# Kernel optimization log

Hardware: AMD Instinct MI355X
Metric: run time of the kernel (lower is better)

## Reference

```python
import jax, jax.numpy as jnp
import numpy as np
from jax import lax

B, NQ, DQ, DKV = 4, 256, 256, 256
H_IMG, W_IMG = 256, 256
HEADS, DH, TOPW, WS, FACTOR = 8, 32, 4, 8, 2
INNER = HEADS * DH
DOUT = 256


def _ln(x, g, b, eps=1e-5):
    mu = x.mean(-1, keepdims=True)
    var = ((x - mu) ** 2).mean(-1, keepdims=True)
    return (x - mu) * lax.rsqrt(var + eps) * g + b


def _softmax_one(x, axis):
    x = x - x.max(axis=axis, keepdims=True)
    e = jnp.exp(x)
    return e / (1.0 + e.sum(axis=axis, keepdims=True))


def setup_inputs():
    key = jax.random.key(0)
    ks = jax.random.split(key, 10)
    s = 0.02
    return {
        'query': jax.random.normal(ks[0], (B, NQ, DQ), jnp.float32),
        'image': jax.random.normal(ks[1], (B, DKV, H_IMG, W_IMG), jnp.float32),
        'conv_w': jax.random.normal(ks[2], (INNER, DKV, FACTOR, FACTOR), jnp.float32) * s,
        'conv_b': jnp.zeros((INNER,), jnp.float32),
        'key_pos_embed': jax.random.normal(ks[3], (1, TOPW * WS * WS, INNER), jnp.float32),
        'normq_g': jnp.ones((DQ,), jnp.float32),
        'normq_b': jnp.zeros((DQ,), jnp.float32),
        'normkv_g': jnp.ones((INNER,), jnp.float32),
        'normkv_b': jnp.zeros((INNER,), jnp.float32),
        'wq': jax.random.normal(ks[4], (INNER, DQ), jnp.float32) * s,
        'wk': jax.random.normal(ks[5], (INNER, INNER), jnp.float32) * s,
        'wv': jax.random.normal(ks[6], (INNER, INNER), jnp.float32) * s,
        'w_rec': jax.random.normal(ks[7], (DQ, INNER), jnp.float32) * s,
        'mlp_g': jnp.ones((DQ,), jnp.float32),
        'mlp_b': jnp.zeros((DQ,), jnp.float32),
        'mlp_w1': jax.random.normal(ks[8], (DOUT, DQ), jnp.float32) * s,
        'mlp_b1': jnp.zeros((DOUT,), jnp.float32),
        'mlp_w2': jax.random.normal(ks[9], (DOUT, DOUT), jnp.float32) * s,
        'mlp_b2': jnp.zeros((DOUT,), jnp.float32),
    }


def reference(query, image, conv_w, conv_b, key_pos_embed, normq_g, normq_b,
              normkv_g, normkv_b, wq, wk, wv, w_rec, mlp_g, mlp_b,
              mlp_w1, mlp_b1, mlp_w2, mlp_b2):
    # 1) patchify image: Conv2d(dim_kv -> inner_dim, k=factor, s=factor)
    imagec = lax.conv_general_dilated(image, conv_w, (FACTOR, FACTOR), 'VALID',
                                      dimension_numbers=('NCHW', 'OIHW', 'NCHW'))
    imagec = imagec + conv_b[None, :, None, None]
    b, c, H, W = imagec.shape
    M, N = H // WS, W // WS  # number of windows per axis
    # einops 'b c (h m) (w n) -> (b m n) (h w) c' with h=w=WS -> DILATED windows
    x = imagec.reshape(b, c, WS, M, WS, N).transpose(0, 3, 5, 2, 4, 1)
    x = x.reshape(b * M * N, WS * WS, c)  # (bMN, ws^2, inner)
    # 2) double softmax_one window pooling
    cor = jnp.einsum('wpc,wqc->wpq', x, x) * (DKV ** -0.5)
    cor = _softmax_one(cor, -1).sum(axis=1)          # (bMN, ws^2)
    cor = _softmax_one(cor, -1)[..., None]           # (bMN, ws^2, 1)
    imagew = (x * cor).sum(axis=1).reshape(b, M * N, c)  # window summaries
    # 3) query projection + top-w window routing (non-differentiable)
    q = _ln(query, normq_g, normq_b) @ wq.T          # (b, Nq, inner)
    rattn = jnp.einsum('bqc,bmc->bqm', lax.stop_gradient(q),
                       lax.stop_gradient(imagew)) * (INNER ** -0.5)
    topw_idx = lax.top_k(rattn, TOPW)[1]             # (b, Nq, topw)
    # 4) gather proposal KV windows
    win_kv = x.reshape(b, M * N, WS * WS, c)
    props = jax.vmap(lambda img, idx: img[idx])(win_kv, topw_idx)  # (b,Nq,topw,ws^2,c)
    nq = q.shape[1]
    props = props.reshape(b * nq, TOPW * WS * WS, c) + key_pos_embed
    # 5) per-query single-token attention over topw*ws^2 keys
    kv = _ln(props, normkv_g, normkv_b)
    k = (kv @ wk.T).reshape(b * nq, -1, HEADS, DH)
    v = (kv @ wv.T).reshape(b * nq, -1, HEADS, DH)
    qh = q.reshape(b * nq, HEADS, DH)
    dots = jnp.einsum('bgc,bngc->bgn', qh, k) * (DH ** -0.5)
    attn = jax.nn.softmax(dots, axis=-1)
    out = jnp.einsum('bgn,bngc->bgc', attn, v).reshape(b, nq, INNER)
    out = out @ w_rec.T + query
    # 6) residual MLP (LN -> Linear -> ReLU -> Linear)
    h = _ln(out, mlp_g, mlp_b)
    h = jax.nn.relu(h @ mlp_w1.T + mlp_b1) @ mlp_w2.T + mlp_b2
    return out + h
```

## Files before the change

kernel.cpp:

```cpp
#include <hip/hip_runtime.h>
#include <math.h>


typedef __bf16 bf16x8_t __attribute__((ext_vector_type(8)));
typedef float f32x4 __attribute__((ext_vector_type(4)));
typedef unsigned short ushortx8 __attribute__((ext_vector_type(8)));
typedef unsigned short ushortx4 __attribute__((ext_vector_type(4)));

__device__ __forceinline__ unsigned short f2bf(float f) {
  unsigned int u = __float_as_uint(f);
  unsigned int r = (u + 0x7FFFu + ((u >> 16) & 1u)) >> 16;
  return (unsigned short)r;
}
__device__ __forceinline__ float bf2f(unsigned short h) {
  return __uint_as_float(((unsigned int)h) << 16);
}

#define MFMA16(a, b, c) \
  __builtin_amdgcn_mfma_f32_16x16x32_bf16( \
      __builtin_bit_cast(bf16x8_t, (a)), __builtin_bit_cast(bf16x8_t, (b)), (c), 0, 0, 0)

__global__ __launch_bounds__(256) void k_prepw(
    const float* __restrict__ cw, unsigned short* __restrict__ cwh,
    unsigned short* __restrict__ cwl)
{
  const int o = blockIdx.x;
  const int k4 = threadIdx.x * 4;
  const float4 w = *(const float4*)(cw + (size_t)o * 1024 + k4);
  float f[4] = {w.x, w.y, w.z, w.w};
  ushortx4 h, l;
#pragma unroll
  for (int i = 0; i < 4; ++i) {
    h[i] = f2bf(f[i]);
    l[i] = f2bf(f[i] - bf2f(h[i]));
  }
  *(ushortx4*)(cwh + (size_t)o * 1024 + k4) = h;
  *(ushortx4*)(cwl + (size_t)o * 1024 + k4) = l;
}

__global__ __launch_bounds__(512, 4) void k_conv(
    const float* __restrict__ img, const unsigned short* __restrict__ cwh,
    const unsigned short* __restrict__ cwl, const float* __restrict__ cb,
    float* __restrict__ x)
{
  __shared__ unsigned short Ah[128 * 40];
  __shared__ unsigned short Al[128 * 40];
  __shared__ unsigned short Bh[128 * 40];
  __shared__ unsigned short Bl[128 * 40];

  const int tid = threadIdx.x;
  const int blk = blockIdx.x;
  const int nh = blk & 1, by = blk >> 1;
  const int b = by >> 7, y = by & 127;
  const int n0 = nh * 128;

  const int lane = tid & 63, wid = tid >> 6;
  const int wr = wid >> 2, wc = wid & 3;
  const int lr = lane & 15, lk = lane >> 4;

  const int ax = tid & 127, aq = tid >> 7;
  const float* abase = img + (size_t)b * 16777216 + (size_t)(2 * y) * 256 + 2 * ax;
  const int bo = tid >> 2, bkq = tid & 3;

  f32x4 acc[4][2];
#pragma unroll
  for (int i = 0; i < 4; ++i)
#pragma unroll
    for (int j = 0; j < 2; ++j) acc[i][j] = (f32x4){0.f, 0.f, 0.f, 0.f};

  for (int kc = 0; kc < 32; ++kc) {
    __syncthreads();
    {
      float f[8];
#pragma unroll
      for (int cc = 0; cc < 2; ++cc) {
        const int cin = kc * 8 + aq * 2 + cc;
        const float* p = abase + (size_t)cin * 65536;
        const float2 v0 = *(const float2*)p;
        const float2 v1 = *(const float2*)(p + 256);
        f[cc * 4 + 0] = v0.x; f[cc * 4 + 1] = v0.y;
        f[cc * 4 + 2] = v1.x; f[cc * 4 + 3] = v1.y;
      }
      ushortx8 h, l;
#pragma unroll
      for (int i = 0; i < 8; ++i) {
        h[i] = f2bf(f[i]);
        l[i] = f2bf(f[i] - bf2f(h[i]));
      }
      *(ushortx8*)&Ah[ax * 40 + aq * 8] = h;
      *(ushortx8*)&Al[ax * 40 + aq * 8] = l;
    }
    {
      const size_t goff = (size_t)(n0 + bo) * 1024 + kc * 32 + bkq * 8;
      *(ushortx8*)&Bh[bo * 40 + bkq * 8] = *(const ushortx8*)(cwh + goff);
      *(ushortx8*)&Bl[bo * 40 + bkq * 8] = *(const ushortx8*)(cwl + goff);
    }
    __syncthreads();
    ushortx8 bh2[2], bl2[2];
#pragma unroll
    for (int ni = 0; ni < 2; ++ni) {
      const int col = wc * 32 + ni * 16 + lr;
      bh2[ni] = *(ushortx8*)&Bh[col * 40 + lk * 8];
      bl2[ni] = *(ushortx8*)&Bl[col * 40 + lk * 8];
    }
#pragma unroll
    for (int mi = 0; mi < 4; ++mi) {
      const int row = wr * 64 + mi * 16 + lr;
      const ushortx8 ah = *(ushortx8*)&Ah[row * 40 + lk * 8];
      const ushortx8 al = *(ushortx8*)&Al[row * 40 + lk * 8];
#pragma unroll
      for (int ni = 0; ni < 2; ++ni) {
        acc[mi][ni] = MFMA16(ah, bh2[ni], acc[mi][ni]);
        acc[mi][ni] = MFMA16(al, bh2[ni], acc[mi][ni]);
        acc[mi][ni] = MFMA16(ah, bl2[ni], acc[mi][ni]);
      }
    }
  }
  const int hh = y >> 4, mm = y & 15;
#pragma unroll
  for (int mi = 0; mi < 4; ++mi) {
    const int pbase = wr * 64 + mi * 16 + lk * 4;
#pragma unroll
    for (int ni = 0; ni < 2; ++ni) {
      const int c = n0 + wc * 32 + ni * 16 + lr;
      const float cbv = cb[c];
#pragma unroll
      for (int r = 0; r < 4; ++r) {
        const int p = pbase + r;
        const int w = p >> 4, n = p & 15;
        const int bwin = b * 256 + mm * 16 + n;
        const int t = hh * 8 + w;
        x[(size_t)(bwin * 64 + t) * 256 + c] = acc[mi][ni][r] + cbv;
      }
    }
  }
}

__global__ __launch_bounds__(256) void k_winpool(
    const float* __restrict__ x, float* __restrict__ imagew)
{
  __shared__ float Xs[64][132];
  __shared__ float cor[64][65];
  __shared__ float wgt[64];
  const int bwin = blockIdx.x;
  const int tid = threadIdx.x;
  const int ty = tid >> 4, tx = tid & 15;
  const float* xw = x + (size_t)bwin * 16384;

  float acc[4][4];
#pragma unroll
  for (int i = 0; i < 4; ++i)
#pragma unroll
    for (int j = 0; j < 4; ++j) acc[i][j] = 0.f;

  for (int half = 0; half < 2; ++half) {
    {
      const int t = tid >> 2, c4 = tid & 3;
      const float* src = xw + t * 256 + half * 128;
#pragma unroll
      for (int i = 0; i < 8; ++i) {
        const int chunk = c4 + 4 * i;
        *(float4*)&Xs[t][chunk * 4] = *(const float4*)(src + chunk * 4);
      }
    }
    __syncthreads();
    for (int c = 0; c < 128; c += 4) {
      float4 av[4], bv[4];
#pragma unroll
      for (int i = 0; i < 4; ++i) av[i] = *(const float4*)&Xs[ty + 16 * i][c];
#pragma unroll
      for (int j = 0; j < 4; ++j) bv[j] = *(const float4*)&Xs[tx + 16 * j][c];
#pragma unroll
      for (int i = 0; i < 4; ++i)
#pragma unroll
        for (int j = 0; j < 4; ++j)
          acc[i][j] += av[i].x * bv[j].x + av[i].y * bv[j].y +
                       av[i].z * bv[j].z + av[i].w * bv[j].w;
    }
    __syncthreads();
  }
  const float sc = 0.0625f;
#pragma unroll
  for (int i = 0; i < 4; ++i)
#pragma unroll
    for (int j = 0; j < 4; ++j) cor[ty + 16 * i][tx + 16 * j] = acc[i][j] * sc;
  __syncthreads();
  if (tid < 64) {
    const int p = tid;
    float m = -INFINITY;
    for (int qq = 0; qq < 64; ++qq) m = fmaxf(m, cor[p][qq]);
    float s = 0.f;
    for (int qq = 0; qq < 64; ++qq) { const float e = expf(cor[p][qq] - m); cor[p][qq] = e; s += e; }
    const float inv = 1.f / (1.f + s);
    for (int qq = 0; qq < 64; ++qq) cor[p][qq] *= inv;
  }
  __syncthreads();
  if (tid < 64) {
    const int qq = tid;
    float s = 0.f;
    for (int p = 0; p < 64; ++p) s += cor[p][qq];
    float m = s;
#pragma unroll
    for (int o = 1; o < 64; o <<= 1) m = fmaxf(m, __shfl_xor(m, o));
    const float e = expf(s - m);
    float tsum = e;
#pragma unroll
    for (int o = 1; o < 64; o <<= 1) tsum += __shfl_xor(tsum, o);
    wgt[qq] = e / (1.f + tsum);
  }
  __syncthreads();
  {
    const int c = tid;
    float a = 0.f;
    for (int qq = 0; qq < 64; ++qq) a += wgt[qq] * xw[qq * 256 + c];
    imagew[(size_t)bwin * 256 + c] = a;
  }
}

__global__ __launch_bounds__(256) void k_ln(
    const float* __restrict__ in, const float* __restrict__ g,
    const float* __restrict__ bb, float* __restrict__ out)
{
  const int row = blockIdx.x, tid = threadIdx.x;
  const float v = in[(size_t)row * 256 + tid];
  float s = v, s2 = v * v;
#pragma unroll
  for (int o = 1; o < 64; o <<= 1) { s += __shfl_xor(s, o); s2 += __shfl_xor(s2, o); }
  __shared__ float ps[4], ps2[4];
  if ((tid & 63) == 0) { ps[tid >> 6] = s; ps2[tid >> 6] = s2; }
  __syncthreads();
  const float S = ps[0] + ps[1] + ps[2] + ps[3];
  const float S2 = ps2[0] + ps2[1] + ps2[2] + ps2[3];
  const float mu = S * (1.f / 256.f);
  const float rs = rsqrtf(S2 * (1.f / 256.f) - mu * mu + 1e-5f);
  out[(size_t)row * 256 + tid] = (v - mu) * rs * g[tid] + bb[tid];
}

template <bool BIAS, bool RELU, bool RES>
__global__ __launch_bounds__(256) void k_gemm(
    const float* __restrict__ A, const float* __restrict__ B,
    const float* __restrict__ bias, const float* __restrict__ res,
    float* __restrict__ C, int M, int N, int K, float scale,
    long aZ, long bZ, long cZ)
{
  A += (size_t)blockIdx.z * aZ;
  B += (size_t)blockIdx.z * bZ;
  C += (size_t)blockIdx.z * cZ;
  const float* R = RES ? res + (size_t)blockIdx.z * cZ : nullptr;
  __shared__ float As[32][65], Bs[32][65];
  const int m0 = blockIdx.x * 64, n0 = blockIdx.y * 64;
  const int tid = threadIdx.x;
  const int ty = tid >> 4, tx = tid & 15;
  const int r = tid >> 3, gq = tid & 7;
  float acc[4][4];
#pragma unroll
  for (int i = 0; i < 4; ++i)
#pragma unroll
    for (int j = 0; j < 4; ++j) acc[i][j] = 0.f;

  for (int kc = 0; kc < K; kc += 32) {
#pragma unroll
    for (int hf = 0; hf < 2; ++hf) {
      const int row = r + hf * 32;
      const float4 va = *(const float4*)(A + (size_t)(m0 + row) * K + kc + gq * 4);
      As[gq * 4 + 0][row] = va.x; As[gq * 4 + 1][row] = va.y;
      As[gq * 4 + 2][row] = va.z; As[gq * 4 + 3][row] = va.w;
      const float4 vb = *(const float4*)(B + (size_t)(n0 + row) * K + kc + gq * 4);
      Bs[gq * 4 + 0][row] = vb.x; Bs[gq * 4 + 1][row] = vb.y;
      Bs[gq * 4 + 2][row] = vb.z; Bs[gq * 4 + 3][row] = vb.w;
    }
    __syncthreads();
#pragma unroll
    for (int kk = 0; kk < 32; ++kk) {
      float a[4], bb2[4];
#pragma unroll
      for (int i = 0; i < 4; ++i) a[i] = As[kk][ty + 16 * i];
#pragma unroll
      for (int j = 0; j < 4; ++j) bb2[j] = Bs[kk][tx + 16 * j];
#pragma unroll
      for (int i = 0; i < 4; ++i)
#pragma unroll
        for (int j = 0; j < 4; ++j) acc[i][j] += a[i] * bb2[j];
    }
    __syncthreads();
  }
#pragma unroll
  for (int i = 0; i < 4; ++i) {
    const int mi = m0 + ty + 16 * i;
#pragma unroll
    for (int j = 0; j < 4; ++j) {
      const int nj = n0 + tx + 16 * j;
      float v = acc[i][j] * scale;
      if (BIAS) v += bias[nj];
      if (RELU) v = fmaxf(v, 0.f);
      if (RES) v += R[(size_t)mi * N + nj];
      C[(size_t)mi * N + nj] = v;
    }
  }
}

__global__ __launch_bounds__(256) void k_topk(
    const float* __restrict__ rattn, int* __restrict__ outi)
{
  const int pair = blockIdx.x * 4 + (threadIdx.x >> 6);
  const int lane = threadIdx.x & 63;
  const float* rp = rattn + (size_t)pair * 256;
  float v[4];
#pragma unroll
  for (int i = 0; i < 4; ++i) v[i] = rp[i * 64 + lane];
  int selmask = 0;
  for (int rsel = 0; rsel < 4; ++rsel) {
    float bv = -INFINITY; int bi = 1 << 30;
#pragma unroll
    for (int i = 0; i < 4; ++i) {
      if (!(selmask & (1 << i))) {
        const float val = v[i]; const int idx = i * 64 + lane;
        if (val > bv || (val == bv && idx < bi)) { bv = val; bi = idx; }
      }
    }
#pragma unroll
    for (int o = 1; o < 64; o <<= 1) {
      const float ov = __shfl_xor(bv, o); const int oi = __shfl_xor(bi, o);
      if (ov > bv || (ov == bv && oi < bi)) { bv = ov; bi = oi; }
    }
    if (lane == 0) outi[pair * 4 + rsel] = bi;
    if (lane == (bi & 63)) selmask |= 1 << (bi >> 6);
  }
}

__global__ __launch_bounds__(256) void k_attn(
    const float* __restrict__ qp, const int* __restrict__ topidx,
    const float* __restrict__ x, const float* __restrict__ pos,
    const float* __restrict__ nkg, const float* __restrict__ nkb,
    const float* __restrict__ wk, const float* __restrict__ wvT,
    float* __restrict__ attnout)
{
  __shared__ float qrow[256];
  __shared__ float qWg[8][260];
  __shared__ float Raw[32][260];
  __shared__ float pooled[8][256];
  __shared__ float dts[8][32];
  __shared__ float muT[32], rsT[32];
  __shared__ float Gh[8], qWb[8], mh[8], lh[8], S1[8], scl[8];

  const int bq = blockIdx.x;
  const int b = bq >> 8;
  const int tid = threadIdx.x;

  qrow[tid] = qp[(size_t)bq * 256 + tid];
#pragma unroll
  for (int h = 0; h < 8; ++h) pooled[h][tid] = 0.f;
  if (tid < 8) { Gh[tid] = 0.f; qWb[tid] = 0.f; mh[tid] = -INFINITY; lh[tid] = 0.f; S1[tid] = 0.f; }
  __syncthreads();

  {
    const float qs = 0.17677669529663689f;
    const float gc = nkg[tid], bc = nkb[tid];
    const int ch = tid >> 2, lo = tid & 3;
    const int off = (((ch & 7) << 3) | (ch >> 3)) * 4 + lo;
#pragma unroll
    for (int h = 0; h < 8; ++h) {
      float a = 0.f;
#pragma unroll
      for (int j = 0; j < 32; ++j)
        a += qrow[h * 32 + j] * wk[(size_t)(h * 32 + j) * 256 + tid];
      a *= qs;
      qWg[h][off] = a * gc;
      float v1 = a * gc, v2 = a * bc;
#pragma unroll
      for (int o = 1; o < 64; o <<= 1) { v1 += __shfl_xor(v1, o); v2 += __shfl_xor(v2, o); }
      if ((tid & 63) == 0) { atomicAdd(&Gh[h], v1); atomicAdd(&qWb[h], v2); }
    }
  }
  __syncthreads();

  for (int tile = 0; tile < 8; ++tile) {
    const int w = tile >> 1, th = tile & 1;
    const int win = topidx[bq * 4 + w];
    {
      const int tt = tid >> 3, c8 = tid & 7;
      const float* xs = x + ((size_t)(b * 256 + win) * 64 + th * 32 + tt) * 256;
      const float* ps = pos + (size_t)(w * 64 + th * 32 + tt) * 256;
      float s = 0.f, s2 = 0.f;
#pragma unroll
      for (int i = 0; i < 8; ++i) {
        const int ck = c8 + 8 * i;
        float4 v = *(const float4*)(xs + ck * 4);
        const float4 p4 = *(const float4*)(ps + ck * 4);
        v.x += p4.x; v.y += p4.y; v.z += p4.z; v.w += p4.w;
        *(float4*)&Raw[tt][ck * 4] = v;
        s += v.x + v.y + v.z + v.w;
        s2 += v.x * v.x + v.y * v.y + v.z * v.z + v.w * v.w;
      }
#pragma unroll
      for (int o = 1; o < 8; o <<= 1) { s += __shfl_xor(s, o); s2 += __shfl_xor(s2, o); }
      if (c8 == 0) {
        const float mu = s * (1.f / 256.f);
        muT[tt] = mu;
        rsT[tt] = rsqrtf(s2 * (1.f / 256.f) - mu * mu + 1e-5f);
      }
    }
    __syncthreads();
    {
      const int tt = tid >> 3, cq = tid & 7;
      float ds[8];
#pragma unroll
      for (int h = 0; h < 8; ++h) ds[h] = 0.f;
#pragma unroll
      for (int ch = 0; ch < 8; ++ch) {
        const float4 rv = *(const float4*)&Raw[tt][cq * 32 + ch * 4];
#pragma unroll
        for (int h = 0; h < 8; ++h) {
          const float4 qv = *(const float4*)&qWg[h][32 * ch + 4 * cq];
          ds[h] += rv.x * qv.x + rv.y * qv.y + rv.z * qv.z + rv.w * qv.w;
        }
      }
#pragma unroll
      for (int o = 1; o < 8; o <<= 1)
#pragma unroll
        for (int h = 0; h < 8; ++h) ds[h] += __shfl_xor(ds[h], o);
      if (cq == 0) {
        const float rs = rsT[tt], mu = muT[tt];
#pragma unroll
        for (int h = 0; h < 8; ++h)
          dts[h][tt] = rs * ds[h] - rs * mu * Gh[h] + qWb[h];
      }
    }
    __syncthreads();
    {
      const int h = tid >> 5, tt = tid & 31;
      const float d = dts[h][tt];
      float tm = d;
#pragma unroll
      for (int o = 1; o < 32; o <<= 1) tm = fmaxf(tm, __shfl_xor(tm, o));
      const float mold = mh[h];
      const float mnew = fmaxf(mold, tm);
      const float e = expf(d - mnew);
      const float wE = e * rsT[tt];
      dts[h][tt] = wE;
      float s1 = e, s2 = wE * muT[tt];
#pragma unroll
      for (int o = 1; o < 32; o <<= 1) { s1 += __shfl_xor(s1, o); s2 += __shfl_xor(s2, o); }
      if (tt == 0) {
        const float f = expf(mold - mnew);
        lh[h] = lh[h] * f + s1;
        S1[h] = S1[h] * f + s2;
        mh[h] = mnew;
        scl[h] = f;
      }
    }
    __syncthreads();
    {
      const int h = tid >> 5, cg = tid & 31;
      const float f = scl[h];
#pragma unroll
      for (int rep = 0; rep < 2; ++rep) {
        const int c = cg * 4 + rep * 128;
        float4 p = *(const float4*)&pooled[h][c];
        p.x *= f; p.y *= f; p.z *= f; p.w *= f;
#pragma unroll 8
        for (int t2 = 0; t2 < 32; ++t2) {
          const float wE = dts[h][t2];
          const float4 rv = *(const float4*)&Raw[t2][c];
          p.x += wE * rv.x; p.y += wE * rv.y; p.z += wE * rv.z; p.w += wE * rv.w;
        }
        *(float4*)&pooled[h][c] = p;
      }
    }
    __syncthreads();
  }
  {
    const int h = tid >> 5, cg = tid & 31;
    const float linv = 1.f / lh[h];
    const float s1v = S1[h];
#pragma unroll
    for (int rep = 0; rep < 8; ++rep) {
      const int c = cg + rep * 32;
      pooled[h][c] = nkg[c] * (pooled[h][c] - s1v) * linv + nkb[c];
    }
  }
  __syncthreads();
  {
    const int j = tid, h = j >> 5;
    float a = 0.f;
    for (int c = 0; c < 256; ++c)
      a += pooled[h][c] * wvT[(size_t)c * 256 + j];
    attnout[(size_t)bq * 256 + j] = a;
  }
}

__global__ void k_transpose256(const float* __restrict__ in, float* __restrict__ out)
{
  __shared__ float tile[32][33];
  const int bx = blockIdx.x * 32, by = blockIdx.y * 32;
  const int tx = threadIdx.x, ty = threadIdx.y;
#pragma unroll
  for (int i = 0; i < 32; i += 8)
    tile[ty + i][tx] = in[(size_t)(by + ty + i) * 256 + bx + tx];
  __syncthreads();
#pragma unroll
  for (int i = 0; i < 32; i += 8)
    out[(size_t)(bx + ty + i) * 256 + by + tx] = tile[tx][ty + i];
}

extern "C" void kernel_launch(void* const* d_in, const int* in_sizes, int n_in,
                              void* d_out, int out_size, void* d_ws, size_t ws_size,
                              hipStream_t stream)
{
  const float* query   = (const float*)d_in[0];
  const float* image   = (const float*)d_in[1];
  const float* conv_w  = (const float*)d_in[2];
  const float* conv_b  = (const float*)d_in[3];
  const float* pos     = (const float*)d_in[4];
  const float* normq_g = (const float*)d_in[5];
  const float* normq_b = (const float*)d_in[6];
  const float* normkv_g= (const float*)d_in[7];
  const float* normkv_b= (const float*)d_in[8];
  const float* wq      = (const float*)d_in[9];
  const float* wk      = (const float*)d_in[10];
  const float* wv      = (const float*)d_in[11];
  const float* w_rec   = (const float*)d_in[12];
  const float* mlp_g   = (const float*)d_in[13];
  const float* mlp_b   = (const float*)d_in[14];
  const float* mlp_w1  = (const float*)d_in[15];
  const float* mlp_b1  = (const float*)d_in[16];
  const float* mlp_w2  = (const float*)d_in[17];
  const float* mlp_b2  = (const float*)d_in[18];
  float* out = (float*)d_out;

  float* ws = (float*)d_ws;
  float* x      = ws;
  float* imagew = x + 16777216;
  float* qln    = imagew + 262144;
  float* qproj  = qln + 262144;
  float* rattn  = qproj + 262144;
  float* attno  = rattn + 262144;
  float* outmid = attno + 262144;
  float* mlpln  = outmid + 262144;
  float* h1     = mlpln + 262144;
  float* wvT    = h1 + 262144;
  int*   topidx = (int*)(wvT + 65536);
  unsigned short* cwh = (unsigned short*)rattn;
  unsigned short* cwl = cwh + 262144;

  k_prepw<<<256, 256, 0, stream>>>(conv_w, cwh, cwl);
  k_conv<<<1024, 512, 0, stream>>>(image, cwh, cwl, conv_b, x);
  k_transpose256<<<dim3(8, 8), dim3(32, 8), 0, stream>>>(wv, wvT);
  k_winpool<<<1024, 256, 0, stream>>>(x, imagew);
  k_ln<<<1024, 256, 0, stream>>>(query, normq_g, normq_b, qln);
  k_gemm<false, false, false><<<dim3(16, 4, 1), 256, 0, stream>>>(
      qln, wq, nullptr, nullptr, qproj, 1024, 256, 256, 1.f, 0, 0, 0);
  k_gemm<false, false, false><<<dim3(4, 4, 4), 256, 0, stream>>>(
      qproj, imagew, nullptr, nullptr, rattn, 256, 256, 256, 0.0625f,
      65536, 65536, 65536);
  k_topk<<<256, 256, 0, stream>>>(rattn, topidx);
  k_attn<<<1024, 256, 0, stream>>>(qproj, topidx, x, pos, normkv_g, normkv_b,
                                   wk, wvT, attno);
  k_gemm<false, false, true><<<dim3(16, 4, 1), 256, 0, stream>>>(
      attno, w_rec, nullptr, query, outmid, 1024, 256, 256, 1.f, 0, 0, 0);
  k_ln<<<1024, 256, 0, stream>>>(outmid, mlp_g, mlp_b, mlpln);
  k_gemm<true, true, false><<<dim3(16, 4, 1), 256, 0, stream>>>(
      mlpln, mlp_w1, mlp_b1, nullptr, h1, 1024, 256, 256, 1.f, 0, 0, 0);
  k_gemm<true, false, true><<<dim3(16, 4, 1), 256, 0, stream>>>(
      h1, mlp_w2, mlp_b2, outmid, out, 1024, 256, 256, 1.f, 0, 0, 0);
}
```

Baseline: 741.8 us.

## Retile conv to 4 waves, parallelise winpool softmax, shrink GEMM M-tile

The patchify conv kernel drops from 512 to 256 threads, so each wave computes a 64x64 tile with a 4x4 accumulator grid and each thread loads float4 image rows. The winpool double-softmax now spreads its row and column reductions across all 256 threads with partial-sum scratch, where before only 64 threads did the work. The small fp32 GEMM uses 32-row M tiles so twice as many blocks launch on the small matrices. Together these trade more registers per wave in the conv, and more syncs in winpool, for better MFMA reuse and higher parallelism.

New measurement: 706.1 us. -4.8%, faster.

```diff
diff --git a/kernel.cpp b/kernel.cpp
--- a/kernel.cpp
+++ b/kernel.cpp
@@ -38,7 +38,7 @@
   *(ushortx4*)(cwl + (size_t)o * 1024 + k4) = l;
 }
 
-__global__ __launch_bounds__(512, 4) void k_conv(
+__global__ __launch_bounds__(256) void k_conv(
     const float* __restrict__ img, const unsigned short* __restrict__ cwh,
     const unsigned short* __restrict__ cwl, const float* __restrict__ cb,
     float* __restrict__ x)
@@ -55,53 +55,59 @@
   const int n0 = nh * 128;
 
   const int lane = tid & 63, wid = tid >> 6;
-  const int wr = wid >> 2, wc = wid & 3;
+  const int wr = wid >> 1, wc = wid & 1;
   const int lr = lane & 15, lk = lane >> 4;
 
-  const int ax = tid & 127, aq = tid >> 7;
-  const float* abase = img + (size_t)b * 16777216 + (size_t)(2 * y) * 256 + 2 * ax;
-  const int bo = tid >> 2, bkq = tid & 3;
-
-  f32x4 acc[4][2];
+  const int r2 = tid & 63, g = tid >> 6;
+  const float* abase = img + (size_t)b * 16777216 + (size_t)(2 * y) * 256 + 4 * r2;
+  const int bcol = tid >> 1, bkq = tid & 1;
+
+  f32x4 acc[4][4];
 #pragma unroll
   for (int i = 0; i < 4; ++i)
 #pragma unroll
-    for (int j = 0; j < 2; ++j) acc[i][j] = (f32x4){0.f, 0.f, 0.f, 0.f};
+    for (int j = 0; j < 4; ++j) acc[i][j] = (f32x4){0.f, 0.f, 0.f, 0.f};
 
   for (int kc = 0; kc < 32; ++kc) {
     __syncthreads();
     {
-      float f[8];
+      float fr0[8], fr1[8];
 #pragma unroll
       for (int cc = 0; cc < 2; ++cc) {
-        const int cin = kc * 8 + aq * 2 + cc;
+        const int cin = kc * 8 + g * 2 + cc;
         const float* p = abase + (size_t)cin * 65536;
-        const float2 v0 = *(const float2*)p;
-        const float2 v1 = *(const float2*)(p + 256);
-        f[cc * 4 + 0] = v0.x; f[cc * 4 + 1] = v0.y;
-        f[cc * 4 + 2] = v1.x; f[cc * 4 + 3] = v1.y;
-      }
-      ushortx8 h, l;
+        const float4 v0 = *(const float4*)p;
+        const float4 v1 = *(const float4*)(p + 256);
+        fr0[cc * 4 + 0] = v0.x; fr0[cc * 4 + 1] = v0.y;
+        fr0[cc * 4 + 2] = v1.x; fr0[cc * 4 + 3] = v1.y;
+        fr1[cc * 4 + 0] = v0.z; fr1[cc * 4 + 1] = v0.w;
+        fr1[cc * 4 + 2] = v1.z; fr1[cc * 4 + 3] = v1.w;
+      }
+      ushortx8 h0, l0, h1, l1;
 #pragma unroll
       for (int i = 0; i < 8; ++i) {
-        h[i] = f2bf(f[i]);
-        l[i] = f2bf(f[i] - bf2f(h[i]));
-      }
-      *(ushortx8*)&Ah[ax * 40 + aq * 8] = h;
-      *(ushortx8*)&Al[ax * 40 + aq * 8] = l;
-    }
-    {
-      const size_t goff = (size_t)(n0 + bo) * 1024 + kc * 32 + bkq * 8;
-      *(ushortx8*)&Bh[bo * 40 + bkq * 8] = *(const ushortx8*)(cwh + goff);
-      *(ushortx8*)&Bl[bo * 40 + bkq * 8] = *(const ushortx8*)(cwl + goff);
-    }
-    __syncthreads();
-    ushortx8 bh2[2], bl2[2];
-#pragma unroll
-    for (int ni = 0; ni < 2; ++ni) {
-      const int col = wc * 32 + ni * 16 + lr;
-      bh2[ni] = *(ushortx8*)&Bh[col * 40 + lk * 8];
-      bl2[ni] = *(ushortx8*)&Bl[col * 40 + lk * 8];
+        h0[i] = f2bf(fr0[i]); l0[i] = f2bf(fr0[i] - bf2f(h0[i]));
+        h1[i] = f2bf(fr1[i]); l1[i] = f2bf(fr1[i] - bf2f(h1[i]));
+      }
+      *(ushortx8*)&Ah[(2 * r2 + 0) * 40 + g * 8] = h0;
+      *(ushortx8*)&Al[(2 * r2 + 0) * 40 + g * 8] = l0;
+      *(ushortx8*)&Ah[(2 * r2 + 1) * 40 + g * 8] = h1;
+      *(ushortx8*)&Al[(2 * r2 + 1) * 40 + g * 8] = l1;
+    }
+    {
+      const size_t goff = (size_t)(n0 + bcol) * 1024 + kc * 32 + bkq * 16;
+      *(ushortx8*)&Bh[bcol * 40 + bkq * 16 + 0] = *(const ushortx8*)(cwh + goff);
+      *(ushortx8*)&Bh[bcol * 40 + bkq * 16 + 8] = *(const ushortx8*)(cwh + goff + 8);
+      *(ushortx8*)&Bl[bcol * 40 + bkq * 16 + 0] = *(const ushortx8*)(cwl + goff);
+      *(ushortx8*)&Bl[bcol * 40 + bkq * 16 + 8] = *(const ushortx8*)(cwl + goff + 8);
+    }
+    __syncthreads();
+    ushortx8 bh4[4], bl4[4];
+#pragma unroll
+    for (int ni = 0; ni < 4; ++ni) {
+      const int col = wc * 64 + ni * 16 + lr;
+      bh4[ni] = *(ushortx8*)&Bh[col * 40 + lk * 8];
+      bl4[ni] = *(ushortx8*)&Bl[col * 40 + lk * 8];
     }
 #pragma unroll
     for (int mi = 0; mi < 4; ++mi) {
@@ -109,10 +115,10 @@
       const ushortx8 ah = *(ushortx8*)&Ah[row * 40 + lk * 8];
       const ushortx8 al = *(ushortx8*)&Al[row * 40 + lk * 8];
 #pragma unroll
-      for (int ni = 0; ni < 2; ++ni) {
-        acc[mi][ni] = MFMA16(ah, bh2[ni], acc[mi][ni]);
-        acc[mi][ni] = MFMA16(al, bh2[ni], acc[mi][ni]);
-        acc[mi][ni] = MFMA16(ah, bl2[ni], acc[mi][ni]);
+      for (int ni = 0; ni < 4; ++ni) {
+        acc[mi][ni] = MFMA16(ah, bh4[ni], acc[mi][ni]);
+        acc[mi][ni] = MFMA16(al, bh4[ni], acc[mi][ni]);
+        acc[mi][ni] = MFMA16(ah, bl4[ni], acc[mi][ni]);
       }
     }
   }
@@ -121,8 +127,8 @@
   for (int mi = 0; mi < 4; ++mi) {
     const int pbase = wr * 64 + mi * 16 + lk * 4;
 #pragma unroll
-    for (int ni = 0; ni < 2; ++ni) {
-      const int c = n0 + wc * 32 + ni * 16 + lr;
+    for (int ni = 0; ni < 4; ++ni) {
+      const int c = n0 + wc * 64 + ni * 16 + lr;
       const float cbv = cb[c];
 #pragma unroll
       for (int r = 0; r < 4; ++r) {
@@ -141,6 +147,7 @@
 {
   __shared__ float Xs[64][132];
   __shared__ float cor[64][65];
+  __shared__ float part[4][64];
   __shared__ float wgt[64];
   const int bwin = blockIdx.x;
   const int tid = threadIdx.x;
@@ -185,20 +192,45 @@
 #pragma unroll
     for (int j = 0; j < 4; ++j) cor[ty + 16 * i][tx + 16 * j] = acc[i][j] * sc;
   __syncthreads();
-  if (tid < 64) {
-    const int p = tid;
+  const int p = tid & 63, q4 = tid >> 6;
+  {
     float m = -INFINITY;
-    for (int qq = 0; qq < 64; ++qq) m = fmaxf(m, cor[p][qq]);
+#pragma unroll
+    for (int i = 0; i < 16; ++i) m = fmaxf(m, cor[p][q4 * 16 + i]);
+    part[q4][p] = m;
+  }
+  __syncthreads();
+  {
+    const float M = fmaxf(fmaxf(part[0][p], part[1][p]),
+                          fmaxf(part[2][p], part[3][p]));
     float s = 0.f;
-    for (int qq = 0; qq < 64; ++qq) { const float e = expf(cor[p][qq] - m); cor[p][qq] = e; s += e; }
-    const float inv = 1.f / (1.f + s);
-    for (int qq = 0; qq < 64; ++qq) cor[p][qq] *= inv;
+#pragma unroll
+    for (int i = 0; i < 16; ++i) {
+      const float e = expf(cor[p][q4 * 16 + i] - M);
+      cor[p][q4 * 16 + i] = e; s += e;
+    }
+    __syncthreads();
+    part[q4][p] = s;
+  }
+  __syncthreads();
+  {
+    const float S = part[0][p] + part[1][p] + part[2][p] + part[3][p];
+    const float inv = 1.f / (1.f + S);
+#pragma unroll
+    for (int i = 0; i < 16; ++i) cor[p][q4 * 16 + i] *= inv;
+  }
+  __syncthreads();
+  {
+    const int q = tid & 63, p4 = tid >> 6;
+    float s = 0.f;
+#pragma unroll
+    for (int i = 0; i < 16; ++i) s += cor[p4 * 16 + i][q];
+    part[p4][q] = s;
   }
   __syncthreads();
   if (tid < 64) {
     const int qq = tid;
-    float s = 0.f;
-    for (int p = 0; p < 64; ++p) s += cor[p][qq];
+    float s = part[0][qq] + part[1][qq] + part[2][qq] + part[3][qq];
     float m = s;
 #pragma unroll
     for (int o = 1; o < 64; o <<= 1) m = fmaxf(m, __shfl_xor(m, o));
@@ -247,45 +279,47 @@
   B += (size_t)blockIdx.z * bZ;
   C += (size_t)blockIdx.z * cZ;
   const float* R = RES ? res + (size_t)blockIdx.z * cZ : nullptr;
-  __shared__ float As[32][65], Bs[32][65];
-  const int m0 = blockIdx.x * 64, n0 = blockIdx.y * 64;
+  __shared__ float As[32][33], Bs[32][65];
+  const int m0 = blockIdx.x * 32, n0 = blockIdx.y * 64;
   const int tid = threadIdx.x;
   const int ty = tid >> 4, tx = tid & 15;
-  const int r = tid >> 3, gq = tid & 7;
-  float acc[4][4];
-#pragma unroll
-  for (int i = 0; i < 4; ++i)
+  const int ar = tid >> 3, ag = tid & 7;
+  const int br = tid >> 2, bg = tid & 3;
+  float acc[2][4];
+#pragma unroll
+  for (int i = 0; i < 2; ++i)
 #pragma unroll
     for (int j = 0; j < 4; ++j) acc[i][j] = 0.f;
 
   for (int kc = 0; kc < K; kc += 32) {
-#pragma unroll
-    for (int hf = 0; hf < 2; ++hf) {
-      const int row = r + hf * 32;
-      const float4 va = *(const float4*)(A + (size_t)(m0 + row) * K + kc + gq * 4);
-      As[gq * 4 + 0][row] = va.x; As[gq * 4 + 1][row] = va.y;
-      As[gq * 4 + 2][row] = va.z; As[gq * 4 + 3][row] = va.w;
-      const float4 vb = *(const float4*)(B + (size_t)(n0 + row) * K + kc + gq * 4);
-      Bs[gq * 4 + 0][row] = vb.x; Bs[gq * 4 + 1][row] = vb.y;
-      Bs[gq * 4 + 2][row] = vb.z; Bs[gq * 4 + 3][row] = vb.w;
+    {
+      const float4 va = *(const float4*)(A + (size_t)(m0 + ar) * K + kc + ag * 4);
+      As[ag * 4 + 0][ar] = va.x; As[ag * 4 + 1][ar] = va.y;
+      As[ag * 4 + 2][ar] = va.z; As[ag * 4 + 3][ar] = va.w;
+      const float4 vb0 = *(const float4*)(B + (size_t)(n0 + br) * K + kc + bg * 8);
+      const float4 vb1 = *(const float4*)(B + (size_t)(n0 + br) * K + kc + bg * 8 + 4);
+      Bs[bg * 8 + 0][br] = vb0.x; Bs[bg * 8 + 1][br] = vb0.y;
+      Bs[bg * 8 + 2][br] = vb0.z; Bs[bg * 8 + 3][br] = vb0.w;
+      Bs[bg * 8 + 4][br] = vb1.x; Bs[bg * 8 + 5][br] = vb1.y;
+      Bs[bg * 8 + 6][br] = vb1.z; Bs[bg * 8 + 7][br] = vb1.w;
     }
     __syncthreads();
 #pragma unroll
     for (int kk = 0; kk < 32; ++kk) {
-      float a[4], bb2[4];
-#pragma unroll
-      for (int i = 0; i < 4; ++i) a[i] = As[kk][ty + 16 * i];
+      float a[2], bb2[4];
+#pragma unroll
+      for (int i = 0; i < 2; ++i) a[i] = As[kk][ty + 16 * i];
 #pragma unroll
       for (int j = 0; j < 4; ++j) bb2[j] = Bs[kk][tx + 16 * j];
 #pragma unroll
-      for (int i = 0; i < 4; ++i)
+      for (int i = 0; i < 2; ++i)
 #pragma unroll
         for (int j = 0; j < 4; ++j) acc[i][j] += a[i] * bb2[j];
     }
     __syncthreads();
   }
 #pragma unroll
-  for (int i = 0; i < 4; ++i) {
+  for (int i = 0; i < 2; ++i) {
     const int mi = m0 + ty + 16 * i;
 #pragma unroll
     for (int j = 0; j < 4; ++j) {
@@ -544,23 +578,23 @@
   unsigned short* cwl = cwh + 262144;
 
   k_prepw<<<256, 256, 0, stream>>>(conv_w, cwh, cwl);
-  k_conv<<<1024, 512, 0, stream>>>(image, cwh, cwl, conv_b, x);
+  k_conv<<<1024, 256, 0, stream>>>(image, cwh, cwl, conv_b, x);
   k_transpose256<<<dim3(8, 8), dim3(32, 8), 0, stream>>>(wv, wvT);
   k_winpool<<<1024, 256, 0, stream>>>(x, imagew);
   k_ln<<<1024, 256, 0, stream>>>(query, normq_g, normq_b, qln);
-  k_gemm<false, false, false><<<dim3(16, 4, 1), 256, 0, stream>>>(
+  k_gemm<false, false, false><<<dim3(32, 4, 1), 256, 0, stream>>>(
       qln, wq, nullptr, nullptr, qproj, 1024, 256, 256, 1.f, 0, 0, 0);
-  k_gemm<false, false, false><<<dim3(4, 4, 4), 256, 0, stream>>>(
+  k_gemm<false, false, false><<<dim3(8, 4, 4), 256, 0, stream>>>(
       qproj, imagew, nullptr, nullptr, rattn, 256, 256, 256, 0.0625f,
       65536, 65536, 65536);
   k_topk<<<256, 256, 0, stream>>>(rattn, topidx);
   k_attn<<<1024, 256, 0, stream>>>(qproj, topidx, x, pos, normkv_g, normkv_b,
                                    wk, wvT, attno);
-  k_gemm<false, false, true><<<dim3(16, 4, 1), 256, 0, stream>>>(
+  k_gemm<false, false, true><<<dim3(32, 4, 1), 256, 0, stream>>>(
       attno, w_rec, nullptr, query, outmid, 1024, 256, 256, 1.f, 0, 0, 0);
   k_ln<<<1024, 256, 0, stream>>>(outmid, mlp_g, mlp_b, mlpln);
-  k_gemm<true, true, false><<<dim3(16, 4, 1), 256, 0, stream>>>(
+  k_gemm<true, true, false><<<dim3(32, 4, 1), 256, 0, stream>>>(
       mlpln, mlp_w1, mlp_b1, nullptr, h1, 1024, 256, 256, 1.f, 0, 0, 0);
-  k_gemm<true, false, true><<<dim3(16, 4, 1), 256, 0, stream>>>(
+  k_gemm<true, false, true><<<dim3(32, 4, 1), 256, 0, stream>>>(
       h1, mlp_w2, mlp_b2, outmid, out, 1024, 256, 256, 1.f, 0, 0, 0);
 }
```
